# Optimization experiments

Measured on AMD Instinct MI355X. Metric: run time of the kernel, lower is better.

## Reference

```python
import jax, jax.numpy as jnp
import numpy as np

B, S, CL, DIM, HEADS, FFN = 2, 2048, 512, 2048, 16, 8192
EPS = 1e-6


def rms_norm(x, w):
    return x * jax.lax.rsqrt(jnp.mean(x * x, axis=-1, keepdims=True) + EPS) * w


def mha(q, k, v, num_heads):
    b, sq, d = q.shape
    sk = k.shape[1]
    hd = d // num_heads
    q = q.reshape(b, sq, num_heads, hd)
    k = k.reshape(b, sk, num_heads, hd)
    v = v.reshape(b, sk, num_heads, hd)
    attn = jnp.einsum('bqhd,bkhd->bhqk', q, k) * (hd ** -0.5)
    attn = jax.nn.softmax(attn, axis=-1)
    out = jnp.einsum('bhqk,bkhd->bqhd', attn, v)
    return out.reshape(b, sq, d)


def setup_inputs() -> dict:
    key = jax.random.key(0)
    ks = iter(jax.random.split(key, 48))
    nrm = lambda shape, scale: jax.random.normal(next(ks), shape, jnp.float32) * scale
    w_scale = DIM ** -0.5
    inp = {
        'x': nrm((B, S, DIM), 1.0),
        'e': nrm((B, 6, DIM), 0.5),
        'context': nrm((B, CL, DIM), 1.0),
        'modulation': nrm((1, 6, DIM), w_scale),
        'norm1_w': jnp.ones((DIM,), jnp.float32),
        'norm2_w': jnp.ones((DIM,), jnp.float32),
        'norm3_w': jnp.ones((DIM,), jnp.float32),
        'sa_nq_w': jnp.ones((DIM,), jnp.float32),
        'sa_nk_w': jnp.ones((DIM,), jnp.float32),
        'ffn_norm_w': jnp.ones((DIM,), jnp.float32),
        'sa_qw': nrm((DIM, DIM), w_scale), 'sa_qb': jnp.zeros((DIM,), jnp.float32),
        'sa_kw': nrm((DIM, DIM), w_scale), 'sa_kb': jnp.zeros((DIM,), jnp.float32),
        'sa_vw': nrm((DIM, DIM), w_scale), 'sa_vb': jnp.zeros((DIM,), jnp.float32),
        'sa_ow': nrm((DIM, DIM), w_scale), 'sa_ob': jnp.zeros((DIM,), jnp.float32),
        'ca_qw': nrm((DIM, DIM), w_scale), 'ca_qb': jnp.zeros((DIM,), jnp.float32),
        'ca_kw': nrm((DIM, DIM), w_scale), 'ca_kb': jnp.zeros((DIM,), jnp.float32),
        'ca_vw': nrm((DIM, DIM), w_scale), 'ca_vb': jnp.zeros((DIM,), jnp.float32),
        'ca_ow': nrm((DIM, DIM), w_scale), 'ca_ob': jnp.zeros((DIM,), jnp.float32),
        'ffn_w1': nrm((DIM, FFN), w_scale), 'ffn_b1': jnp.zeros((FFN,), jnp.float32),
        'ffn_w2': nrm((FFN, DIM), FFN ** -0.5), 'ffn_b2': jnp.zeros((DIM,), jnp.float32),
    }
    return inp


def reference(x, e, context, modulation, norm1_w, norm2_w, norm3_w, sa_nq_w, sa_nk_w,
              ffn_norm_w, sa_qw, sa_qb, sa_kw, sa_kb, sa_vw, sa_vb, sa_ow, sa_ob,
              ca_qw, ca_qb, ca_kw, ca_kb, ca_vw, ca_vb, ca_ow, ca_ob,
              ffn_w1, ffn_b1, ffn_w2, ffn_b2):
    # AdaLN modulation: (modulation + e) chunked into 6 along dim=1 -> each [B,1,DIM]
    mod = modulation + e
    e0, e1, e2, e3, e4, e5 = [mod[:, i:i + 1, :] for i in range(6)]

    # --- self attention with qk_norm=True ---
    h = rms_norm(x, norm1_w) * (1.0 + e1) + e0
    q = rms_norm(h @ sa_qw + sa_qb, sa_nq_w)
    k = rms_norm(h @ sa_kw + sa_kb, sa_nk_w)
    v = h @ sa_vw + sa_vb
    y = mha(q, k, v, HEADS) @ sa_ow + sa_ob
    x = x + y * e2

    # --- cross attention (cross_attn_norm=False, no qk norm) ---
    h = rms_norm(x, norm2_w)
    q = h @ ca_qw + ca_qb
    k = context @ ca_kw + ca_kb
    v = context @ ca_vw + ca_vb
    y = mha(q, k, v, HEADS) @ ca_ow + ca_ob
    x = x + y

    # --- FFN: modulate(norm3(x)) -> RMSNorm -> Linear -> GELU(tanh) -> Linear ---
    h = rms_norm(x, norm3_w) * (1.0 + e4) + e3
    h = rms_norm(h, ffn_norm_w)
    h = jax.nn.gelu(h @ ffn_w1 + ffn_b1, approximate=True)
    y = h @ ffn_w2 + ffn_b2
    x = x + y * e5
    return x
```

## Files before the change

kernel.cpp:

```cpp
#include <hip/hip_runtime.h>
#include <hip/hip_bf16.h>
#include <cstdint>

#define DIM   2048
#define HEADS 16
#define HD    128
#define SEQ   2048
#define CLEN  512
#define FFND  8192
#define BATCH 2

using bf16 = __hip_bfloat16;
typedef __attribute__((ext_vector_type(8))) short  short8;
typedef __attribute__((ext_vector_type(4))) short  short4v;
typedef __attribute__((ext_vector_type(4))) float  f32x4;
typedef __attribute__((ext_vector_type(8))) __bf16 bf16x8;

__device__ __forceinline__ short f2bs(float f){ bf16 h = __float2bfloat16(f); return __builtin_bit_cast(short, h); }
__device__ __forceinline__ float bs2f(short s){ return __builtin_bit_cast(float, (uint32_t)((uint16_t)s) << 16); }

__device__ __forceinline__ f32x4 mfma16(short8 a, short8 b, f32x4 c){
  return __builtin_amdgcn_mfma_f32_16x16x32_bf16(
      __builtin_bit_cast(bf16x8, a), __builtin_bit_cast(bf16x8, b), c, 0, 0, 0);
}

__device__ __forceinline__ void gload_lds16(const void* g, const void* l){
  __builtin_amdgcn_global_load_lds(
      (const __attribute__((address_space(1))) void*)(uintptr_t)g,
      (__attribute__((address_space(3))) void*)(uint32_t)(uintptr_t)l, 16, 0, 0);
}

__device__ __forceinline__ float block_sum(float v, float* sbuf, int tid){
  #pragma unroll
  for (int m = 32; m >= 1; m >>= 1) v += __shfl_xor(v, m, 64);
  const int w = tid >> 6;
  if ((tid & 63) == 0) sbuf[w] = v;
  __syncthreads();
  float r = sbuf[0] + sbuf[1] + sbuf[2] + sbuf[3];
  __syncthreads();
  return r;
}


__global__ void modadd_k(const float* __restrict__ m, const float* __restrict__ e,
                         float* __restrict__ out){
  int i = blockIdx.x * 256 + threadIdx.x;
  out[i] = m[i % (6 * DIM)] + e[i];
}

__global__ void f2b8_k(const float* __restrict__ in, bf16* __restrict__ out){
  int i = blockIdx.x * 256 + threadIdx.x;
  const float4* p = (const float4*)in;
  float4 a = p[2*i], c = p[2*i+1];
  short8 o;
  o[0]=f2bs(a.x); o[1]=f2bs(a.y); o[2]=f2bs(a.z); o[3]=f2bs(a.w);
  o[4]=f2bs(c.x); o[5]=f2bs(c.y); o[6]=f2bs(c.z); o[7]=f2bs(c.w);
  *((short8*)out + i) = o;
}

__global__ __launch_bounds__(256) void transpose_w(const float* __restrict__ W,
                                                   bf16* __restrict__ Wt, int K, int N){
  __shared__ float tile[32][33];
  const int tx = threadIdx.x & 31, ty = threadIdx.x >> 5;
  const size_t k0 = blockIdx.y * 32, n0 = blockIdx.x * 32;
  #pragma unroll
  for (int i = 0; i < 4; i++)
    tile[ty + i*8][tx] = W[(k0 + ty + i*8) * (size_t)N + n0 + tx];
  __syncthreads();
  #pragma unroll
  for (int i = 0; i < 4; i++)
    Wt[(n0 + ty + i*8) * (size_t)K + k0 + tx] = __float2bfloat16(tile[tx][ty + i*8]);
}

template<int MODE>
__global__ __launch_bounds__(256) void norm_x(const float* __restrict__ x,
    const float* __restrict__ w1, const float* __restrict__ w2,
    const float* __restrict__ mod, bf16* __restrict__ out, int S)
{
  const int row = blockIdx.x, tid = threadIdx.x;
  const int b = row / S;
  __shared__ float sbuf[4];
  const float* xr = x + (size_t)row * DIM;
  float v[8];
  #pragma unroll
  for (int i = 0; i < 2; i++){
    float4 t = *(const float4*)(xr + i*1024 + tid*4);
    v[i*4+0]=t.x; v[i*4+1]=t.y; v[i*4+2]=t.z; v[i*4+3]=t.w;
  }
  float ss = 0.f;
  #pragma unroll
  for (int j = 0; j < 8; j++) ss += v[j]*v[j];
  ss = block_sum(ss, sbuf, tid);
  const float r = rsqrtf(ss * (1.0f/DIM) + 1e-6f);
  const float* mb = mod + (size_t)b * 6 * DIM;
  float t8[8];
  #pragma unroll
  for (int i = 0; i < 2; i++)
    #pragma unroll
    for (int j = 0; j < 4; j++){
      int n = i*1024 + tid*4 + j;
      float val = v[i*4+j] * r * w1[n];
      if (MODE == 1) val = val * (1.f + mb[DIM + n]) + mb[n];
      if (MODE == 3) val = val * (1.f + mb[4*DIM + n]) + mb[3*DIM + n];
      t8[i*4+j] = val;
    }
  if (MODE == 3){
    float s2 = 0.f;
    #pragma unroll
    for (int j = 0; j < 8; j++) s2 += t8[j]*t8[j];
    s2 = block_sum(s2, sbuf, tid);
    const float r2 = rsqrtf(s2 * (1.0f/DIM) + 1e-6f);
    #pragma unroll
    for (int i = 0; i < 2; i++)
      #pragma unroll
      for (int j = 0; j < 4; j++){
        int n = i*1024 + tid*4 + j;
        t8[i*4+j] = t8[i*4+j] * r2 * w2[n];
      }
  }
  #pragma unroll
  for (int i = 0; i < 2; i++){
    short4v o;
    #pragma unroll
    for (int j = 0; j < 4; j++) o[j] = f2bs(t8[i*4+j]);
    *(short4v*)(out + (size_t)row*DIM + i*1024 + tid*4) = o;
  }
}

__global__ __launch_bounds__(256) void rmsnorm_bf16_ip(bf16* __restrict__ x,
                                                       const float* __restrict__ w){
  const int row = blockIdx.x, tid = threadIdx.x;
  __shared__ float sbuf[4];
  bf16* xr = x + (size_t)row * DIM;
  short8 v = *(const short8*)(xr + tid*8);
  float f[8]; float ss = 0.f;
  #pragma unroll
  for (int j = 0; j < 8; j++){ f[j] = bs2f(v[j]); ss += f[j]*f[j]; }
  ss = block_sum(ss, sbuf, tid);
  const float r = rsqrtf(ss * (1.0f/DIM) + 1e-6f);
  short8 o;
  #pragma unroll
  for (int j = 0; j < 8; j++) o[j] = f2bs(f[j] * r * w[tid*8 + j]);
  *(short8*)(xr + tid*8) = o;
}

#define GBUF 24576
template<int EPI>
__global__ __launch_bounds__(512, 2) void gemm_bf16(
    const bf16* __restrict__ A, const bf16* __restrict__ Bt,
    const float* __restrict__ bias, const float* __restrict__ xin,
    const float* __restrict__ mod, float* __restrict__ outf,
    bf16* __restrict__ outb, int M, int N, int K, int S_tok, int eidx)
{
  __shared__ __align__(16) char lds[3][GBUF];
  const int tid = threadIdx.x;
  const int w = tid >> 6, l = tid & 63;
  const int lrow = l & 15, lhi = l >> 4;
  const int wm = w >> 2, wn = w & 3;
  const size_t m0 = (size_t)blockIdx.y * 128, n0 = (size_t)blockIdx.x * 256;

  f32x4 acc[4][4] = {};

  const int srow = tid >> 2, sseg = tid & 3;
  const bf16* gA = A  + (m0 + srow) * (size_t)K + sseg * 8;
  const bf16* gB = Bt + (n0 + srow) * (size_t)K + sseg * 8;
  const size_t bskip = (size_t)128 * K;

  auto stage = [&](int kt, char* buf){
    const size_t ko = (size_t)kt * 32;
    gload_lds16(gA + ko,         buf + tid * 16);
    gload_lds16(gB + ko,         buf + 8192  + tid * 16);
    gload_lds16(gB + ko + bskip, buf + 16384 + tid * 16);
  };

  const int nt = K >> 5;
  stage(0, lds[0]);
  stage(1, lds[1]);
  asm volatile("s_waitcnt vmcnt(3)" ::: "memory");
  __builtin_amdgcn_s_barrier();
  __builtin_amdgcn_sched_barrier(0);

  int bi = 0;
  for (int t = 0; t < nt; ++t){
    const char* br = lds[bi];
    const bool st = (t + 2 < nt);
    if (st){
      int wi = bi + 2; if (wi >= 3) wi -= 3;
      stage(t + 2, lds[wi]);
    }
    short8 af[4], bf[4];
    #pragma unroll
    for (int mi = 0; mi < 4; mi++)
      af[mi] = *(const short8*)(br + (wm*64 + mi*16 + lrow)*64 + lhi*16);
    #pragma unroll
    for (int ni = 0; ni < 4; ni++)
      bf[ni] = *(const short8*)(br + 8192 + (wn*64 + ni*16 + lrow)*64 + lhi*16);
    __builtin_amdgcn_s_setprio(1);
    #pragma unroll
    for (int mi = 0; mi < 4; mi++)
      #pragma unroll
      for (int ni = 0; ni < 4; ni++)
        acc[mi][ni] = mfma16(af[mi], bf[ni], acc[mi][ni]);
    __builtin_amdgcn_s_setprio(0);
    if (st)               { asm volatile("s_waitcnt vmcnt(3)" ::: "memory"); }
    else if (t + 1 < nt)  { asm volatile("s_waitcnt vmcnt(0)" ::: "memory"); }
    __builtin_amdgcn_s_barrier();
    __builtin_amdgcn_sched_barrier(0);
    bi = (bi + 1 == 3) ? 0 : bi + 1;
  }

  #pragma unroll
  for (int mi = 0; mi < 4; mi++)
    #pragma unroll
    for (int ni = 0; ni < 4; ni++)
      #pragma unroll
      for (int r = 0; r < 4; r++){
        const size_t m = m0 + wm*64 + mi*16 + lhi*4 + r;
        const size_t n = n0 + wn*64 + ni*16 + lrow;
        float v = acc[mi][ni][r] + bias[n];
        if constexpr (EPI == 0) {
          outb[m * N + n] = __float2bfloat16(v);
        } else if constexpr (EPI == 1) {
          const size_t b = m / S_tok, s = m % S_tok;
          const size_t h = n >> 7, d = n & 127;
          outb[((b*HEADS + h)*HD + d) * S_tok + s] = __float2bfloat16(v);
        } else if constexpr (EPI == 2) {
          const float ev = mod[(m / S_tok) * 6 * DIM + (size_t)eidx * DIM + n];
          outf[m * N + n] = xin[m * N + n] + v * ev;
        } else if constexpr (EPI == 3) {
          outf[m * N + n] += v;
        } else {
          float u = 0.7978845608028654f * (v + 0.044715f * v * v * v);
          outb[m * N + n] = __float2bfloat16(0.5f * v * (1.0f + tanhf(u)));
        }
      }
}

__global__ __launch_bounds__(256, 2) void attn_fwd(
    const bf16* __restrict__ Q, const bf16* __restrict__ Kp, const bf16* __restrict__ Vt,
    bf16* __restrict__ O, int SQ, int SKV)
{
  const int tid = threadIdx.x, w = tid >> 6, l = tid & 63;
  const int lrow = l & 15, lhi = l >> 4;
  const int nwg = gridDim.x;
  const int p = blockIdx.x;
  const int f = (p & 7) * (nwg >> 3) + (p >> 3);
  const int nqb = SQ >> 6;
  const int xq = f % nqb;
  const int h  = (f / nqb) % HEADS;
  const int b  = f / (nqb * HEADS);
  const int q0 = xq * 64 + w * 16;

  __shared__ __align__(16) char kls[2][16384];
  __shared__ __align__(16) char vls[2][16384];
  __shared__ __align__(16) bf16 P[4][16][72];
  const float scale = 0.08838834764831845f;

  const bf16* qp = Q + ((size_t)(b*SQ + q0 + lrow))*DIM + h*HD + lhi*8;
  short8 qf[4];
  #pragma unroll
  for (int ds = 0; ds < 4; ds++) qf[ds] = *(const short8*)(qp + ds*32);

  const bf16* kg = Kp + (size_t)b*SKV*DIM + h*HD;
  const bf16* vg = Vt + (size_t)(b*HEADS + h)*HD*SKV;

  f32x4 acc[8] = {};
  float m_run = -INFINITY, l_run = 0.f;
  const int nt = SKV >> 6;

  auto stage = [&](int buf, int kv0){
    char* kd = &kls[buf][0];
    #pragma unroll
    for (int i = 0; i < 4; i++){
      int sid = i*256 + tid;
      int row = sid >> 4, sg = sid & 15;
      int gsg = sg ^ (row & 7);
      gload_lds16(kg + (size_t)(kv0 + row)*DIM + gsg*8, kd + sid*16);
    }
    char* vd = &vls[buf][0];
    #pragma unroll
    for (int i = 0; i < 4; i++){
      int sid = i*256 + tid;
      int d = sid >> 3, sg = sid & 7;
      int gsg = sg ^ (d & 7);
      gload_lds16(vg + (size_t)d*SKV + kv0 + gsg*8, vd + sid*16);
    }
  };

  stage(0, 0);
  __syncthreads();

  for (int t = 0; t < nt; ++t){
    if (t + 1 < nt) stage((t + 1) & 1, (t + 1) * 64);
    const char* kb = &kls[t & 1][0];
    const char* vb = &vls[t & 1][0];

    f32x4 st[4] = {};
    #pragma unroll
    for (int kvf = 0; kvf < 4; kvf++){
      const int row = kvf*16 + lrow;
      const int rx = row & 7;
      #pragma unroll
      for (int ds = 0; ds < 4; ds++){
        const int seg = (ds*4 + lhi) ^ rx;
        short8 kf = *(const short8*)(kb + row*256 + seg*16);
        st[kvf] = mfma16(kf, qf[ds], st[kvf]);
      }
    }

    float sv[16]; float smax = -INFINITY;
    #pragma unroll
    for (int kvf = 0; kvf < 4; kvf++)
      #pragma unroll
      for (int r = 0; r < 4; r++){
        float xv = st[kvf][r] * scale;
        sv[kvf*4+r] = xv; smax = fmaxf(smax, xv);
      }
    smax = fmaxf(smax, __shfl_xor(smax, 16, 64));
    smax = fmaxf(smax, __shfl_xor(smax, 32, 64));
    const float mnew = fmaxf(m_run, smax);
    const float corr = __expf(m_run - mnew);
    float psum = 0.f;
    #pragma unroll
    for (int i = 0; i < 16; i++){ float pe = __expf(sv[i] - mnew); sv[i] = pe; psum += pe; }
    psum += __shfl_xor(psum, 16, 64); psum += __shfl_xor(psum, 32, 64);
    l_run = l_run * corr + psum;
    m_run = mnew;

    #pragma unroll
    for (int kvf = 0; kvf < 4; kvf++){
      short4v o;
      #pragma unroll
      for (int r = 0; r < 4; r++) o[r] = f2bs(sv[kvf*4+r]);
      *(short4v*)&P[w][lrow][kvf*16 + lhi*4] = o;
    }

    float cr[4];
    #pragma unroll
    for (int r = 0; r < 4; r++) cr[r] = __shfl(corr, lhi*4 + r, 64);
    #pragma unroll
    for (int df = 0; df < 8; df++){
      acc[df][0] *= cr[0]; acc[df][1] *= cr[1]; acc[df][2] *= cr[2]; acc[df][3] *= cr[3];
    }

    asm volatile("s_waitcnt lgkmcnt(0)" ::: "memory");
    __builtin_amdgcn_sched_barrier(0);

    short8 pf0 = *(const short8*)&P[w][lrow][lhi*8];
    short8 pf1 = *(const short8*)&P[w][lrow][32 + lhi*8];
    #pragma unroll
    for (int df = 0; df < 8; df++){
      const int d = df*16 + lrow;
      const int dx = d & 7;
      short8 vf0 = *(const short8*)(vb + d*128 + ((lhi)     ^ dx)*16);
      short8 vf1 = *(const short8*)(vb + d*128 + ((lhi + 4) ^ dx)*16);
      acc[df] = mfma16(pf0, vf0, acc[df]);
      acc[df] = mfma16(pf1, vf1, acc[df]);
    }
    __syncthreads();
  }

  const float linv = 1.0f / l_run;
  float li[4];
  #pragma unroll
  for (int r = 0; r < 4; r++) li[r] = __shfl(linv, lhi*4 + r, 64);
  #pragma unroll
  for (int df = 0; df < 8; df++)
    #pragma unroll
    for (int r = 0; r < 4; r++){
      const size_t q = q0 + lhi*4 + r;
      O[((size_t)(b*SQ + q))*DIM + h*HD + df*16 + lrow] = __float2bfloat16(acc[df][r] * li[r]);
    }
}


extern "C" void kernel_launch(void* const* d_in, const int* in_sizes, int n_in,
                              void* d_out, int out_size, void* d_ws, size_t ws_size,
                              hipStream_t stream)
{
  const float* x    = (const float*)d_in[0];
  const float* e    = (const float*)d_in[1];
  const float* ctx  = (const float*)d_in[2];
  const float* modw = (const float*)d_in[3];
  const float* n1w  = (const float*)d_in[4];
  const float* n2w  = (const float*)d_in[5];
  const float* n3w  = (const float*)d_in[6];
  const float* nqw  = (const float*)d_in[7];
  const float* nkw  = (const float*)d_in[8];
  const float* fnw  = (const float*)d_in[9];
  const float* saqw = (const float*)d_in[10]; const float* saqb = (const float*)d_in[11];
  const float* sakw = (const float*)d_in[12]; const float* sakb = (const float*)d_in[13];
  const float* savw = (const float*)d_in[14]; const float* savb = (const float*)d_in[15];
  const float* saow = (const float*)d_in[16]; const float* saob = (const float*)d_in[17];
  const float* caqw = (const float*)d_in[18]; const float* caqb = (const float*)d_in[19];
  const float* cakw = (const float*)d_in[20]; const float* cakb = (const float*)d_in[21];
  const float* cavw = (const float*)d_in[22]; const float* cavb = (const float*)d_in[23];
  const float* caow = (const float*)d_in[24]; const float* caob = (const float*)d_in[25];
  const float* fw1  = (const float*)d_in[26]; const float* fb1  = (const float*)d_in[27];
  const float* fw2  = (const float*)d_in[28]; const float* fb2  = (const float*)d_in[29];
  float* out = (float*)d_out;
  (void)in_sizes; (void)n_in; (void)out_size; (void)ws_size;

  char* ws = (char*)d_ws;
  size_t off = 0;
  auto alloc = [&](size_t bytes) -> void* {
    void* p = ws + off; off = (off + bytes + 255) & ~(size_t)255; return p;
  };
  bf16*  wt   = (bf16*)alloc((size_t)FFND * DIM * 2);
  float* mod  = (float*)alloc((size_t)BATCH * 6 * DIM * 4);
  bf16*  ctxb = (bf16*)alloc((size_t)BATCH * CLEN * DIM * 2);
  bf16*  hbuf = (bf16*)alloc((size_t)BATCH * SEQ * DIM * 2);
  bf16*  qbuf = (bf16*)alloc((size_t)BATCH * SEQ * DIM * 2);
  bf16*  kbuf = (bf16*)alloc((size_t)BATCH * SEQ * DIM * 2);
  bf16*  vtb  = (bf16*)alloc((size_t)BATCH * SEQ * DIM * 2);
  bf16*  aout = (bf16*)alloc((size_t)BATCH * SEQ * DIM * 2);
  float* xcur = (float*)alloc((size_t)BATCH * SEQ * DIM * 4);
  bf16*  hf   = (bf16*)alloc((size_t)BATCH * SEQ * FFND * 2);

  const int M = BATCH * SEQ;
  const int Mc = BATCH * CLEN;

  modadd_k<<<dim3(96), dim3(256), 0, stream>>>(modw, e, mod);
  f2b8_k<<<dim3(1024), dim3(256), 0, stream>>>(ctx, ctxb);

  norm_x<1><<<dim3(M), dim3(256), 0, stream>>>(x, n1w, nullptr, mod, hbuf, SEQ);

  transpose_w<<<dim3(DIM/32, DIM/32), dim3(256), 0, stream>>>(saqw, wt, DIM, DIM);
  gemm_bf16<0><<<dim3(DIM/256, M/128), dim3(512), 0, stream>>>(hbuf, wt, saqb, nullptr, mod, nullptr, qbuf, M, DIM, DIM, SEQ, 0);
  rmsnorm_bf16_ip<<<dim3(M), dim3(256), 0, stream>>>(qbuf, nqw);

  transpose_w<<<dim3(DIM/32, DIM/32), dim3(256), 0, stream>>>(sakw, wt, DIM, DIM);
  gemm_bf16<0><<<dim3(DIM/256, M/128), dim3(512), 0, stream>>>(hbuf, wt, sakb, nullptr, mod, nullptr, kbuf, M, DIM, DIM, SEQ, 0);
  rmsnorm_bf16_ip<<<dim3(M), dim3(256), 0, stream>>>(kbuf, nkw);

  transpose_w<<<dim3(DIM/32, DIM/32), dim3(256), 0, stream>>>(savw, wt, DIM, DIM);
  gemm_bf16<1><<<dim3(DIM/256, M/128), dim3(512), 0, stream>>>(hbuf, wt, savb, nullptr, mod, nullptr, vtb, M, DIM, DIM, SEQ, 0);

  attn_fwd<<<dim3((SEQ/64)*HEADS*BATCH), dim3(256), 0, stream>>>(qbuf, kbuf, vtb, aout, SEQ, SEQ);

  transpose_w<<<dim3(DIM/32, DIM/32), dim3(256), 0, stream>>>(saow, wt, DIM, DIM);
  gemm_bf16<2><<<dim3(DIM/256, M/128), dim3(512), 0, stream>>>(aout, wt, saob, x, mod, xcur, nullptr, M, DIM, DIM, SEQ, 2);

  norm_x<2><<<dim3(M), dim3(256), 0, stream>>>(xcur, n2w, nullptr, mod, hbuf, SEQ);

  transpose_w<<<dim3(DIM/32, DIM/32), dim3(256), 0, stream>>>(caqw, wt, DIM, DIM);
  gemm_bf16<0><<<dim3(DIM/256, M/128), dim3(512), 0, stream>>>(hbuf, wt, caqb, nullptr, mod, nullptr, qbuf, M, DIM, DIM, SEQ, 0);

  transpose_w<<<dim3(DIM/32, DIM/32), dim3(256), 0, stream>>>(cakw, wt, DIM, DIM);
  gemm_bf16<0><<<dim3(DIM/256, Mc/128), dim3(512), 0, stream>>>(ctxb, wt, cakb, nullptr, mod, nullptr, kbuf, Mc, DIM, DIM, CLEN, 0);

  transpose_w<<<dim3(DIM/32, DIM/32), dim3(256), 0, stream>>>(cavw, wt, DIM, DIM);
  gemm_bf16<1><<<dim3(DIM/256, Mc/128), dim3(512), 0, stream>>>(ctxb, wt, cavb, nullptr, mod, nullptr, vtb, Mc, DIM, DIM, CLEN, 0);

  attn_fwd<<<dim3((SEQ/64)*HEADS*BATCH), dim3(256), 0, stream>>>(qbuf, kbuf, vtb, aout, SEQ, CLEN);

  transpose_w<<<dim3(DIM/32, DIM/32), dim3(256), 0, stream>>>(caow, wt, DIM, DIM);
  gemm_bf16<3><<<dim3(DIM/256, M/128), dim3(512), 0, stream>>>(aout, wt, caob, nullptr, mod, xcur, nullptr, M, DIM, DIM, SEQ, 0);

  norm_x<3><<<dim3(M), dim3(256), 0, stream>>>(xcur, n3w, fnw, mod, hbuf, SEQ);

  transpose_w<<<dim3(FFND/32, DIM/32), dim3(256), 0, stream>>>(fw1, wt, DIM, FFND);
  gemm_bf16<4><<<dim3(FFND/256, M/128), dim3(512), 0, stream>>>(hbuf, wt, fb1, nullptr, mod, nullptr, hf, M, FFND, DIM, SEQ, 0);

  transpose_w<<<dim3(DIM/32, FFND/32), dim3(256), 0, stream>>>(fw2, wt, FFND, DIM);
  gemm_bf16<2><<<dim3(DIM/256, M/128), dim3(512), 0, stream>>>(hf, wt, fb2, xcur, mod, out, nullptr, M, DIM, FFND, SEQ, 5);
}
```

Before: 976.1 us.

## Use 4-wave GEMM blocks with 128x64 per-wave tiles and XOR-swizzled LDS

Cuts the GEMM block from 8 waves to 4 while keeping the 128x256 block tile, so each wave now computes a 128x64 output tile with 32 MFMA accumulators. The larger per-wave tile raises MFMA work per LDS fragment read. Global-to-LDS staging uses an XOR swizzle on the 16-byte segments, matched on the read side, to reduce LDS bank conflicts. The cost is higher register pressure (128 accumulator floats per lane) and fewer waves per CU to hide latency.

```diff
diff --git a/kernel.cpp b/kernel.cpp
--- a/kernel.cpp
+++ b/kernel.cpp
@@ -146,7 +146,7 @@
 
 #define GBUF 24576
 template<int EPI>
-__global__ __launch_bounds__(512, 2) void gemm_bf16(
+__global__ __launch_bounds__(256, 2) void gemm_bf16(
     const bf16* __restrict__ A, const bf16* __restrict__ Bt,
     const float* __restrict__ bias, const float* __restrict__ xin,
     const float* __restrict__ mod, float* __restrict__ outf,
@@ -154,31 +154,40 @@
 {
   __shared__ __align__(16) char lds[3][GBUF];
   const int tid = threadIdx.x;
-  const int w = tid >> 6, l = tid & 63;
+  const int wn = tid >> 6, l = tid & 63;
   const int lrow = l & 15, lhi = l >> 4;
-  const int wm = w >> 2, wn = w & 3;
   const size_t m0 = (size_t)blockIdx.y * 128, n0 = (size_t)blockIdx.x * 256;
 
-  f32x4 acc[4][4] = {};
-
-  const int srow = tid >> 2, sseg = tid & 3;
-  const bf16* gA = A  + (m0 + srow) * (size_t)K + sseg * 8;
-  const bf16* gB = Bt + (n0 + srow) * (size_t)K + sseg * 8;
-  const size_t bskip = (size_t)128 * K;
+  f32x4 acc[8][4] = {};
+
+  const int sidA0 = tid, sidA1 = tid + 256;
+  const int sidB0 = tid, sidB1 = tid + 256, sidB2 = tid + 512, sidB3 = tid + 768;
+  auto gofs = [&](int sid){ return (size_t)(sid >> 2) * K + (size_t)(((sid & 3) ^ ((sid >> 3) & 3)) * 8); };
+  const bf16* gA0 = A  + m0 * K + gofs(sidA0);
+  const bf16* gA1 = A  + m0 * K + gofs(sidA1);
+  const bf16* gB0 = Bt + n0 * K + gofs(sidB0);
+  const bf16* gB1 = Bt + n0 * K + gofs(sidB1);
+  const bf16* gB2 = Bt + n0 * K + gofs(sidB2);
+  const bf16* gB3 = Bt + n0 * K + gofs(sidB3);
 
   auto stage = [&](int kt, char* buf){
     const size_t ko = (size_t)kt * 32;
-    gload_lds16(gA + ko,         buf + tid * 16);
-    gload_lds16(gB + ko,         buf + 8192  + tid * 16);
-    gload_lds16(gB + ko + bskip, buf + 16384 + tid * 16);
+    gload_lds16(gA0 + ko, buf + sidA0 * 16);
+    gload_lds16(gA1 + ko, buf + sidA1 * 16);
+    gload_lds16(gB0 + ko, buf + 8192 + sidB0 * 16);
+    gload_lds16(gB1 + ko, buf + 8192 + sidB1 * 16);
+    gload_lds16(gB2 + ko, buf + 8192 + sidB2 * 16);
+    gload_lds16(gB3 + ko, buf + 8192 + sidB3 * 16);
   };
 
   const int nt = K >> 5;
   stage(0, lds[0]);
   stage(1, lds[1]);
-  asm volatile("s_waitcnt vmcnt(3)" ::: "memory");
+  asm volatile("s_waitcnt vmcnt(6)" ::: "memory");
   __builtin_amdgcn_s_barrier();
   __builtin_amdgcn_sched_barrier(0);
+
+  const int sread = (lhi ^ ((lrow >> 1) & 3)) * 16;
 
   int bi = 0;
   for (int t = 0; t < nt; ++t){
@@ -188,21 +197,21 @@
       int wi = bi + 2; if (wi >= 3) wi -= 3;
       stage(t + 2, lds[wi]);
     }
-    short8 af[4], bf[4];
-    #pragma unroll
-    for (int mi = 0; mi < 4; mi++)
-      af[mi] = *(const short8*)(br + (wm*64 + mi*16 + lrow)*64 + lhi*16);
+    short8 af[8], bf[4];
+    #pragma unroll
+    for (int mi = 0; mi < 8; mi++)
+      af[mi] = *(const short8*)(br + (mi*16 + lrow)*64 + sread);
     #pragma unroll
     for (int ni = 0; ni < 4; ni++)
-      bf[ni] = *(const short8*)(br + 8192 + (wn*64 + ni*16 + lrow)*64 + lhi*16);
+      bf[ni] = *(const short8*)(br + 8192 + (wn*64 + ni*16 + lrow)*64 + sread);
     __builtin_amdgcn_s_setprio(1);
     #pragma unroll
-    for (int mi = 0; mi < 4; mi++)
+    for (int mi = 0; mi < 8; mi++)
       #pragma unroll
       for (int ni = 0; ni < 4; ni++)
         acc[mi][ni] = mfma16(af[mi], bf[ni], acc[mi][ni]);
     __builtin_amdgcn_s_setprio(0);
-    if (st)               { asm volatile("s_waitcnt vmcnt(3)" ::: "memory"); }
+    if (st)               { asm volatile("s_waitcnt vmcnt(6)" ::: "memory"); }
     else if (t + 1 < nt)  { asm volatile("s_waitcnt vmcnt(0)" ::: "memory"); }
     __builtin_amdgcn_s_barrier();
     __builtin_amdgcn_sched_barrier(0);
@@ -210,12 +219,12 @@
   }
 
   #pragma unroll
-  for (int mi = 0; mi < 4; mi++)
+  for (int mi = 0; mi < 8; mi++)
     #pragma unroll
     for (int ni = 0; ni < 4; ni++)
       #pragma unroll
       for (int r = 0; r < 4; r++){
-        const size_t m = m0 + wm*64 + mi*16 + lhi*4 + r;
+        const size_t m = m0 + mi*16 + lhi*4 + r;
         const size_t n = n0 + wn*64 + ni*16 + lrow;
         float v = acc[mi][ni][r] + bias[n];
         if constexpr (EPI == 0) {
@@ -426,42 +435,42 @@
   norm_x<1><<<dim3(M), dim3(256), 0, stream>>>(x, n1w, nullptr, mod, hbuf, SEQ);
 
   transpose_w<<<dim3(DIM/32, DIM/32), dim3(256), 0, stream>>>(saqw, wt, DIM, DIM);
-  gemm_bf16<0><<<dim3(DIM/256, M/128), dim3(512), 0, stream>>>(hbuf, wt, saqb, nullptr, mod, nullptr, qbuf, M, DIM, DIM, SEQ, 0);
+  gemm_bf16<0><<<dim3(DIM/256, M/128), dim3(256), 0, stream>>>(hbuf, wt, saqb, nullptr, mod, nullptr, qbuf, M, DIM, DIM, SEQ, 0);
   rmsnorm_bf16_ip<<<dim3(M), dim3(256), 0, stream>>>(qbuf, nqw);
 
   transpose_w<<<dim3(DIM/32, DIM/32), dim3(256), 0, stream>>>(sakw, wt, DIM, DIM);
-  gemm_bf16<0><<<dim3(DIM/256, M/128), dim3(512), 0, stream>>>(hbuf, wt, sakb, nullptr, mod, nullptr, kbuf, M, DIM, DIM, SEQ, 0);
+  gemm_bf16<0><<<dim3(DIM/256, M/128), dim3(256), 0, stream>>>(hbuf, wt, sakb, nullptr, mod, nullptr, kbuf, M, DIM, DIM, SEQ, 0);
   rmsnorm_bf16_ip<<<dim3(M), dim3(256), 0, stream>>>(kbuf, nkw);
 
   transpose_w<<<dim3(DIM/32, DIM/32), dim3(256), 0, stream>>>(savw, wt, DIM, DIM);
-  gemm_bf16<1><<<dim3(DIM/256, M/128), dim3(512), 0, stream>>>(hbuf, wt, savb, nullptr, mod, nullptr, vtb, M, DIM, DIM, SEQ, 0);
+  gemm_bf16<1><<<dim3(DIM/256, M/128), dim3(256), 0, stream>>>(hbuf, wt, savb, nullptr, mod, nullptr, vtb, M, DIM, DIM, SEQ, 0);
 
   attn_fwd<<<dim3((SEQ/64)*HEADS*BATCH), dim3(256), 0, stream>>>(qbuf, kbuf, vtb, aout, SEQ, SEQ);
 
   transpose_w<<<dim3(DIM/32, DIM/32), dim3(256), 0, stream>>>(saow, wt, DIM, DIM);
-  gemm_bf16<2><<<dim3(DIM/256, M/128), dim3(512), 0, stream>>>(aout, wt, saob, x, mod, xcur, nullptr, M, DIM, DIM, SEQ, 2);
+  gemm_bf16<2><<<dim3(DIM/256, M/128), dim3(256), 0, stream>>>(aout, wt, saob, x, mod, xcur, nullptr, M, DIM, DIM, SEQ, 2);
 
   norm_x<2><<<dim3(M), dim3(256), 0, stream>>>(xcur, n2w, nullptr, mod, hbuf, SEQ);
 
   transpose_w<<<dim3(DIM/32, DIM/32), dim3(256), 0, stream>>>(caqw, wt, DIM, DIM);
-  gemm_bf16<0><<<dim3(DIM/256, M/128), dim3(512), 0, stream>>>(hbuf, wt, caqb, nullptr, mod, nullptr, qbuf, M, DIM, DIM, SEQ, 0);
+  gemm_bf16<0><<<dim3(DIM/256, M/128), dim3(256), 0, stream>>>(hbuf, wt, caqb, nullptr, mod, nullptr, qbuf, M, DIM, DIM, SEQ, 0);
 
   transpose_w<<<dim3(DIM/32, DIM/32), dim3(256), 0, stream>>>(cakw, wt, DIM, DIM);
-  gemm_bf16<0><<<dim3(DIM/256, Mc/128), dim3(512), 0, stream>>>(ctxb, wt, cakb, nullptr, mod, nullptr, kbuf, Mc, DIM, DIM, CLEN, 0);
+  gemm_bf16<0><<<dim3(DIM/256, Mc/128), dim3(256), 0, stream>>>(ctxb, wt, cakb, nullptr, mod, nullptr, kbuf, Mc, DIM, DIM, CLEN, 0);
 
   transpose_w<<<dim3(DIM/32, DIM/32), dim3(256), 0, stream>>>(cavw, wt, DIM, DIM);
-  gemm_bf16<1><<<dim3(DIM/256, Mc/128), dim3(512), 0, stream>>>(ctxb, wt, cavb, nullptr, mod, nullptr, vtb, Mc, DIM, DIM, CLEN, 0);
+  gemm_bf16<1><<<dim3(DIM/256, Mc/128), dim3(256), 0, stream>>>(ctxb, wt, cavb, nullptr, mod, nullptr, vtb, Mc, DIM, DIM, CLEN, 0);
 
   attn_fwd<<<dim3((SEQ/64)*HEADS*BATCH), dim3(256), 0, stream>>>(qbuf, kbuf, vtb, aout, SEQ, CLEN);
 
   transpose_w<<<dim3(DIM/32, DIM/32), dim3(256), 0, stream>>>(caow, wt, DIM, DIM);
-  gemm_bf16<3><<<dim3(DIM/256, M/128), dim3(512), 0, stream>>>(aout, wt, caob, nullptr, mod, xcur, nullptr, M, DIM, DIM, SEQ, 0);
+  gemm_bf16<3><<<dim3(DIM/256, M/128), dim3(256), 0, stream>>>(aout, wt, caob, nullptr, mod, xcur, nullptr, M, DIM, DIM, SEQ, 0);
 
   norm_x<3><<<dim3(M), dim3(256), 0, stream>>>(xcur, n3w, fnw, mod, hbuf, SEQ);
 
   transpose_w<<<dim3(FFND/32, DIM/32), dim3(256), 0, stream>>>(fw1, wt, DIM, FFND);
-  gemm_bf16<4><<<dim3(FFND/256, M/128), dim3(512), 0, stream>>>(hbuf, wt, fb1, nullptr, mod, nullptr, hf, M, FFND, DIM, SEQ, 0);
+  gemm_bf16<4><<<dim3(FFND/256, M/128), dim3(256), 0, stream>>>(hbuf, wt, fb1, nullptr, mod, nullptr, hf, M, FFND, DIM, SEQ, 0);
 
   transpose_w<<<dim3(DIM/32, FFND/32), dim3(256), 0, stream>>>(fw2, wt, FFND, DIM);
-  gemm_bf16<2><<<dim3(DIM/256, M/128), dim3(512), 0, stream>>>(hf, wt, fb2, xcur, mod, out, nullptr, M, DIM, FFND, SEQ, 5);
-}
+  gemm_bf16<2><<<dim3(DIM/256, M/128), dim3(256), 0, stream>>>(hf, wt, fb2, xcur, mod, out, nullptr, M, DIM, FFND, SEQ, 5);
+}
```

Result: slower. 1.021 ms (+4.6%).
